# Optimization experiments

Measured on AMD Instinct MI355X. Metric: run time of the kernel, lower is better.

## Reference

```python
import math
import jax, jax.numpy as jnp
import numpy as np


def fht(x):
    """Normalized fast Hadamard transform over the last axis (size = power of 2)."""
    n = x.shape[-1]
    pre = x.shape[:-1]
    y = x.reshape(-1, n)
    h = 1
    while h < n:
        y = y.reshape(-1, n // (2 * h), 2, h)
        a = y[:, :, 0, :]
        b = y[:, :, 1, :]
        y = jnp.stack([a + b, a - b], axis=2)
        h *= 2
    return y.reshape(*pre, n) * jnp.float32(1.0 / math.sqrt(n))


def setup_inputs() -> dict:
    key = jax.random.key(0)
    ks = jax.random.split(key, 8)
    B, N, M, G = 8192, 4096, 4096, 512  # tokens, in_features(n_pad), out_features(m_pad), n_pad//8
    CB = 256  # E8 shell codebook entries (8-bit indices), each an 8-dim lattice point
    x = jax.random.normal(ks[0], (B, N), dtype=jnp.float32)
    Qidxs = jax.random.randint(ks[1], (M, G), 0, CB, dtype=jnp.int32)
    Qidxs2 = jax.random.randint(ks[2], (M, G), 0, CB, dtype=jnp.int32)
    SU = jax.random.rademacher(ks[3], (M,), dtype=jnp.float32)  # row sign vector
    SV = jax.random.rademacher(ks[4], (N,), dtype=jnp.float32)  # column sign vector
    codebook = jax.random.normal(ks[5], (CB, 8), dtype=jnp.float32)
    codebook2 = jax.random.normal(ks[6], (CB, 8), dtype=jnp.float32)
    Wscale = jnp.asarray(0.85, dtype=jnp.float32)
    inv_resid_scale = jnp.asarray(0.07, dtype=jnp.float32)  # nonzero -> stage-2 enabled
    return {"x": x, "Qidxs": Qidxs, "Qidxs2": Qidxs2, "SU": SU, "SV": SV,
            "codebook": codebook, "codebook2": codebook2,
            "Wscale": Wscale, "inv_resid_scale": inv_resid_scale}


def reference(x, Qidxs, Qidxs2, SU, SV, codebook, codebook2, Wscale, inv_resid_scale):
    # in_features == n_pad and out_features == m_pad here (powers of 2), so no pad/slice.
    m_pad, g = Qidxs.shape
    n_pad = g * 8
    # 1) input RHT: signs then Hadamard
    x_rht = fht(x * SV[None, :])  # (B, n_pad)
    # 2) dequantize weights in RHT domain: codebook lookup per 8-dim group + residual stage
    W_rht = codebook[Qidxs].reshape(m_pad, n_pad)
    W_rht = W_rht + codebook2[Qidxs2].reshape(m_pad, n_pad) * inv_resid_scale
    # 3) matmul in RHT domain with global scale
    y_rht = (x_rht @ W_rht.T) * Wscale  # (B, m_pad)
    # 4) output inverse RHT: Hadamard then signs
    y = fht(y_rht) * SU[None, :]
    return y
```

## Files before the change

### kernel.cpp

```cpp
#include <hip/hip_runtime.h>

#define B_DIM 8192
#define N_DIM 4096
#define M_DIM 4096
#define G_DIM 512

typedef short bf16x8 __attribute__((ext_vector_type(8)));
typedef float f32x4 __attribute__((ext_vector_type(4)));

typedef __attribute__((address_space(1))) const void gvoid_t;
typedef __attribute__((address_space(3))) void lvoid_t;

__device__ __forceinline__ void load_lds16(const void* g, void* l) {
    __builtin_amdgcn_global_load_lds((gvoid_t*)g, (lvoid_t*)l, 16, 0, 0);
}

__device__ __forceinline__ unsigned lds_u32(const void* p) {
    return (unsigned)(unsigned long long)(lvoid_t*)p;
}

__device__ __forceinline__ unsigned short f2bf(float f) {
    union { float f; unsigned int u; } v; v.f = f;
    unsigned int u = v.u;
    unsigned int r = (u + 0x7fffu + ((u >> 16) & 1u)) >> 16;
    return (unsigned short)r;
}
__device__ __forceinline__ float bf2f(unsigned short s) {
    union { unsigned int u; float f; } v; v.u = ((unsigned int)s) << 16;
    return v.f;
}

__device__ __forceinline__ void h16(float* v) {
#pragma unroll
    for (int h = 1; h < 16; h <<= 1) {
#pragma unroll
        for (int i = 0; i < 16; i++) {
            if (!(i & h)) {
                float a = v[i], b = v[i | h];
                v[i] = a + b;
                v[i | h] = a - b;
            }
        }
    }
}

__device__ __forceinline__ void h64(float* v) {
#pragma unroll
    for (int h = 1; h < 64; h <<= 1) {
#pragma unroll
        for (int i = 0; i < 64; i++) {
            if (!(i & h)) {
                float a = v[i], b = v[i | h];
                v[i] = a + b;
                v[i | h] = a - b;
            }
        }
    }
}

__global__ __launch_bounds__(256) void k_build_w(
    const int* __restrict__ q1, const int* __restrict__ q2,
    const float* __restrict__ cb1, const float* __restrict__ cb2,
    const float* __restrict__ wsp, const float* __restrict__ irsp,
    unsigned short* __restrict__ W) {
    __shared__ float c1[256 * 9];
    __shared__ float c2[256 * 9];
    int t = threadIdx.x;
#pragma unroll
    for (int j = 0; j < 8; j++) {
        c1[t * 9 + j] = cb1[t * 8 + j];
        c2[t * 9 + j] = cb2[t * 8 + j];
    }
    __syncthreads();
    float ws = wsp[0];
    float irs = irsp[0] * ws;
    int gid = blockIdx.x * 256 + t;
    int i1 = q1[gid] * 9;
    int i2 = q2[gid] * 9;
    union { unsigned short s[8]; int4 v; } o;
#pragma unroll
    for (int j = 0; j < 8; j++) {
        o.s[j] = f2bf(c1[i1 + j] * ws + c2[i2 + j] * irs);
    }
    *(int4*)(W + (size_t)gid * 8) = o.v;
}

__global__ __launch_bounds__(256) void k_hadw(
    unsigned short* __restrict__ W, int base_mul, int step, float scale) {
    int c = blockIdx.x * 256 + threadIdx.x;
    int base = blockIdx.y * base_mul;
    float v[64];
#pragma unroll
    for (int j = 0; j < 64; j++)
        v[j] = bf2f(W[(size_t)(base + j * step) * N_DIM + c]);
    h64(v);
#pragma unroll
    for (int j = 0; j < 64; j++)
        W[(size_t)(base + j * step) * N_DIM + c] = f2bf(v[j] * scale);
}

__global__ __launch_bounds__(256) void k_rht_in(
    const float* __restrict__ x, const float* __restrict__ SV,
    unsigned short* __restrict__ out) {
    __shared__ float lds[4352];
    int row = blockIdx.x;
    int t = threadIdx.x;
    const float* xr = x + (size_t)row * N_DIM;
    float v[16];
#pragma unroll
    for (int r = 0; r < 16; r++) {
        int n = t + (r << 8);
        v[r] = xr[n] * SV[n] * 0.015625f;
    }
    h16(v);
#pragma unroll
    for (int r = 0; r < 16; r++) { int n = t + (r << 8); lds[n + (n >> 4)] = v[r]; }
    __syncthreads();
#pragma unroll
    for (int r = 0; r < 16; r++) { int n = (t << 4) + r; v[r] = lds[n + (n >> 4)]; }
    h16(v);
#pragma unroll
    for (int r = 0; r < 16; r++) { int n = (t << 4) + r; lds[n + (n >> 4)] = v[r]; }
    __syncthreads();
#pragma unroll
    for (int r = 0; r < 16; r++) {
        int n = (t & 15) | (r << 4) | ((t >> 4) << 8);
        v[r] = lds[n + (n >> 4)];
    }
    h16(v);
#pragma unroll
    for (int r = 0; r < 16; r++) {
        int n = (t & 15) | (r << 4) | ((t >> 4) << 8);
        lds[n + (n >> 4)] = v[r];
    }
    __syncthreads();
    unsigned short* orow = out + (size_t)row * N_DIM;
#pragma unroll
    for (int r = 0; r < 16; r++) {
        int n = t + (r << 8);
        orow[n] = f2bf(lds[n + (n >> 4)]);
    }
}

#define DSR(D, A, OFF) \
    asm volatile("ds_read_b128 %0, %1 offset:" #OFF : "=v"(D) : "v"(A))
#define SB0() __builtin_amdgcn_sched_barrier(0)
#define SGB(M, N) __builtin_amdgcn_sched_group_barrier((M), (N), 0)

__global__ __launch_bounds__(512, 2) void k_gemm(
    const unsigned short* __restrict__ A,
    const unsigned short* __restrict__ Bw,
    const float* __restrict__ SU,
    float* __restrict__ C) {
    __shared__ __align__(16) unsigned short lds[4 * 16384];

    int t = threadIdx.x;
    int w = t >> 6;
    int l = t & 63;

    int lin = blockIdx.x;
    int xcd = lin & 7;
    int idx = lin >> 3;
    int bn = xcd * 2 + (idx >> 5);
    int bm = idx & 31;

    int lx = l ^ (l >> 3);
    const unsigned short* aS0 =
        A + (size_t)(bm * 256 + w * 16 + (lx >> 2)) * N_DIM + (lx & 3) * 8;
    const unsigned short* aS1 = aS0 + (size_t)128 * N_DIM;
    const unsigned short* bS0 =
        Bw + (size_t)(bn * 256 + w * 16 + (lx >> 2)) * N_DIM + (lx & 3) * 8;
    const unsigned short* bS1 = bS0 + (size_t)128 * N_DIM;

    int wm = w >> 2;
    int wn = w & 3;
    int quad = l >> 4;
    int ln = l & 15;
    unsigned ldsU = lds_u32(lds);
    unsigned aByte = ldsU +
        (unsigned)(((((wm * 128) + ln) << 6) | (quad << 4)) ^ ((ln >> 1) << 4));
    unsigned bByte = ldsU + 16384u +
        (unsigned)(((((wn * 64) + ln) << 6) | (quad << 4)) ^ ((ln >> 1) << 4));

    f32x4 acc[8][4];
#pragma unroll
    for (int i = 0; i < 8; i++)
#pragma unroll
        for (int j = 0; j < 4; j++) {
            f32x4 z = {0.f, 0.f, 0.f, 0.f};
            acc[i][j] = z;
        }

#define STAGE(KT) do {                                              \
        int kt_ = (KT);                                             \
        int ks_ = kt_ < 127 ? kt_ : 127;                            \
        unsigned short* d_ = lds + ((unsigned)kt_ & 3u) * 16384 + w * 512; \
        load_lds16(aS0 + ks_ * 32, d_);                             \
        load_lds16(aS1 + ks_ * 32, d_ + 4096);                      \
        load_lds16(bS0 + ks_ * 32, d_ + 8192);                      \
        load_lds16(bS1 + ks_ * 32, d_ + 12288);                     \
    } while (0)

#define GROUP(I, BC) do {                                           \
        acc[I][0] = __builtin_amdgcn_mfma_f32_16x16x32_bf16(        \
            af[I], BC[0], acc[I][0], 0, 0, 0);                      \
        acc[I][1] = __builtin_amdgcn_mfma_f32_16x16x32_bf16(        \
            af[I], BC[1], acc[I][1], 0, 0, 0);                      \
        acc[I][2] = __builtin_amdgcn_mfma_f32_16x16x32_bf16(        \
            af[I], BC[2], acc[I][2], 0, 0, 0);                      \
        acc[I][3] = __builtin_amdgcn_mfma_f32_16x16x32_bf16(        \
            af[I], BC[3], acc[I][3], 0, 0, 0);                      \
    } while (0)

#define BODY(K, BC, BN) do {                                        \
        asm volatile("s_waitcnt lgkmcnt(0)");                       \
        SB0();   \
        STAGE((K) + 3);                                             \
        unsigned aun = aByte + ((unsigned)((K) + 1) & 3u) * 32768u; \
        unsigned bun = bByte + ((unsigned)((K) + 1) & 3u) * 32768u; \
        SGB(0x10, 4);                       \
        GROUP(0, BC); DSR(af[0], aun, 0);    DSR(BN[0], bun, 0);    \
        SGB(0x8, 4); SGB(0x100, 2);                                 \
        GROUP(1, BC); DSR(af[1], aun, 1024); DSR(BN[1], bun, 1024); \
        SGB(0x8, 4); SGB(0x100, 2);                                 \
        GROUP(2, BC); DSR(af[2], aun, 2048); DSR(BN[2], bun, 2048); \
        SGB(0x8, 4); SGB(0x100, 2);                                 \
        GROUP(3, BC); DSR(af[3], aun, 3072); DSR(BN[3], bun, 3072); \
        SGB(0x8, 4); SGB(0x100, 2);                                 \
        GROUP(4, BC); DSR(af[4], aun, 4096);                        \
        SGB(0x8, 4); SGB(0x100, 1);                                 \
        GROUP(5, BC); DSR(af[5], aun, 5120);                        \
        SGB(0x8, 4); SGB(0x100, 1);                                 \
        GROUP(6, BC); DSR(af[6], aun, 6144);                        \
        SGB(0x8, 4); SGB(0x100, 1);                                 \
        GROUP(7, BC); DSR(af[7], aun, 7168);                        \
        SGB(0x8, 4); SGB(0x100, 1);                                 \
        asm volatile("s_waitcnt vmcnt(4)");   \
        asm volatile("" ::: "memory");                              \
        __builtin_amdgcn_s_barrier();                               \
        asm volatile("" ::: "memory");                              \
    } while (0)

    bf16x8 af[8], bfrA[4], bfrB[4];

    STAGE(0);
    STAGE(1);
    STAGE(2);
    asm volatile("s_waitcnt vmcnt(4)");
    __builtin_amdgcn_s_barrier();
    asm volatile("" ::: "memory");
    {
        unsigned au0 = aByte;
        unsigned bu0 = bByte;
        DSR(af[0], au0, 0);
        DSR(af[1], au0, 1024);
        DSR(af[2], au0, 2048);
        DSR(af[3], au0, 3072);
        DSR(af[4], au0, 4096);
        DSR(af[5], au0, 5120);
        DSR(af[6], au0, 6144);
        DSR(af[7], au0, 7168);
        DSR(bfrA[0], bu0, 0);
        DSR(bfrA[1], bu0, 1024);
        DSR(bfrA[2], bu0, 2048);
        DSR(bfrA[3], bu0, 3072);
    }

    for (int k = 0; k < N_DIM / 32; k += 2) {
        BODY(k, bfrA, bfrB);
        BODY(k + 1, bfrB, bfrA);
    }
    asm volatile("s_waitcnt vmcnt(0) lgkmcnt(0)");

#pragma unroll
    for (int j = 0; j < 4; j++) {
        int col = bn * 256 + wn * 64 + j * 16 + ln;
        float su = SU[col];
#pragma unroll
        for (int i = 0; i < 8; i++) {
#pragma unroll
            for (int r = 0; r < 4; r++) {
                int rowg = bm * 256 + wm * 128 + i * 16 + quad * 4 + r;
                C[(size_t)rowg * M_DIM + col] = acc[i][j][r] * su;
            }
        }
    }
#undef STAGE
#undef GROUP
#undef BODY
}

extern "C" void kernel_launch(void* const* d_in, const int* in_sizes, int n_in,
                              void* d_out, int out_size, void* d_ws, size_t ws_size,
                              hipStream_t stream) {
    const float* x    = (const float*)d_in[0];
    const int*   q1   = (const int*)d_in[1];
    const int*   q2   = (const int*)d_in[2];
    const float* SU   = (const float*)d_in[3];
    const float* SV   = (const float*)d_in[4];
    const float* cb1  = (const float*)d_in[5];
    const float* cb2  = (const float*)d_in[6];
    const float* wsp  = (const float*)d_in[7];
    const float* irsp = (const float*)d_in[8];
    float* out = (float*)d_out;

    unsigned short* xrht = (unsigned short*)d_ws;
    unsigned short* Wb   = xrht + (size_t)B_DIM * N_DIM;

    k_build_w<<<dim3((M_DIM * G_DIM) / 256), dim3(256), 0, stream>>>(
        q1, q2, cb1, cb2, wsp, irsp, Wb);
    k_hadw<<<dim3(N_DIM / 256, 64), dim3(256), 0, stream>>>(Wb, 1, 64, 1.0f);
    k_hadw<<<dim3(N_DIM / 256, 64), dim3(256), 0, stream>>>(Wb, 64, 1, 0.015625f);
    k_rht_in<<<dim3(B_DIM), dim3(256), 0, stream>>>(x, SV, xrht);
    k_gemm<<<dim3(512), dim3(512), 0, stream>>>(xrht, Wb, SU, out);
}
```

Measured before the change: 521.0 us.

## Fuse weight dequant with first Hadamard pass and tile second pass via LDS

Weight construction now dequantizes a 64-row by 256-column tile into shared memory and applies the low-stride 64-point Hadamard there before writing bf16. This removes one full round trip of the weight matrix through global memory. The remaining high-stride Hadamard pass also stages a tile in LDS with 16-byte vector loads and stores instead of per-element 2-byte accesses. The large shared tile reduces occupancy per CU, and the extra intermediate rounding to bf16 between passes is kept.

```diff
diff --git a/kernel.cpp b/kernel.cpp
--- a/kernel.cpp
+++ b/kernel.cpp
@@ -58,13 +58,14 @@
     }
 }
 
-__global__ __launch_bounds__(256) void k_build_w(
+__global__ __launch_bounds__(256) void k_build_hlo(
     const int* __restrict__ q1, const int* __restrict__ q2,
     const float* __restrict__ cb1, const float* __restrict__ cb2,
     const float* __restrict__ wsp, const float* __restrict__ irsp,
     unsigned short* __restrict__ W) {
     __shared__ float c1[256 * 9];
     __shared__ float c2[256 * 9];
+    __shared__ float tile[64 * 256];
     int t = threadIdx.x;
 #pragma unroll
     for (int j = 0; j < 8; j++) {
@@ -74,29 +75,77 @@
     __syncthreads();
     float ws = wsp[0];
     float irs = irsp[0] * ws;
-    int gid = blockIdx.x * 256 + t;
-    int i1 = q1[gid] * 9;
-    int i2 = q2[gid] * 9;
-    union { unsigned short s[8]; int4 v; } o;
-#pragma unroll
-    for (int j = 0; j < 8; j++) {
-        o.s[j] = f2bf(c1[i1 + j] * ws + c2[i2 + j] * irs);
-    }
-    *(int4*)(W + (size_t)gid * 8) = o.v;
-}
-
-__global__ __launch_bounds__(256) void k_hadw(
-    unsigned short* __restrict__ W, int base_mul, int step, float scale) {
-    int c = blockIdx.x * 256 + threadIdx.x;
-    int base = blockIdx.y * base_mul;
-    float v[64];
-#pragma unroll
-    for (int j = 0; j < 64; j++)
-        v[j] = bf2f(W[(size_t)(base + j * step) * N_DIM + c]);
-    h64(v);
-#pragma unroll
-    for (int j = 0; j < 64; j++)
-        W[(size_t)(base + j * step) * N_DIM + c] = f2bf(v[j] * scale);
+    int ct = blockIdx.x;
+    int h  = blockIdx.y;
+    int g0 = ct * 32;
+    int rr = t >> 5;
+    int j  = t & 31;
+#pragma unroll
+    for (int p = 0; p < 8; p++) {
+        int row = rr + 8 * p;
+        int m = 64 * h + row;
+        int i1 = q1[m * G_DIM + g0 + j] * 9;
+        int i2 = q2[m * G_DIM + g0 + j] * 9;
+        float* dst = &tile[row * 256 + 8 * j];
+#pragma unroll
+        for (int i = 0; i < 8; i++) dst[i] = c1[i1 + i] * ws + c2[i2 + i] * irs;
+    }
+    __syncthreads();
+    {
+        float v[64];
+#pragma unroll
+        for (int r2 = 0; r2 < 64; r2++) v[r2] = tile[r2 * 256 + t];
+        h64(v);
+#pragma unroll
+        for (int r2 = 0; r2 < 64; r2++) tile[r2 * 256 + t] = v[r2];
+    }
+    __syncthreads();
+#pragma unroll
+    for (int p = 0; p < 8; p++) {
+        int row = rr + 8 * p;
+        int m = 64 * h + row;
+        union { unsigned short s[8]; int4 v4; } o;
+#pragma unroll
+        for (int i = 0; i < 8; i++) o.s[i] = f2bf(tile[row * 256 + 8 * j + i]);
+        *(int4*)(W + (size_t)m * N_DIM + ct * 256 + 8 * j) = o.v4;
+    }
+}
+
+__global__ __launch_bounds__(256) void k_hadw_hi(unsigned short* __restrict__ W) {
+    __shared__ float tile[64 * 256];
+    int t = threadIdx.x;
+    int ct = blockIdx.x;
+    int lo = blockIdx.y;
+    int rr = t >> 5;
+    int j = t & 31;
+#pragma unroll
+    for (int p = 0; p < 8; p++) {
+        int hi = rr + 8 * p;
+        size_t m = (size_t)lo + 64 * hi;
+        union { int4 v4; unsigned short s[8]; } u;
+        u.v4 = *(const int4*)(W + m * N_DIM + ct * 256 + 8 * j);
+#pragma unroll
+        for (int i = 0; i < 8; i++) tile[hi * 256 + 8 * j + i] = bf2f(u.s[i]);
+    }
+    __syncthreads();
+    {
+        float v[64];
+#pragma unroll
+        for (int hi = 0; hi < 64; hi++) v[hi] = tile[hi * 256 + t];
+        h64(v);
+#pragma unroll
+        for (int hi = 0; hi < 64; hi++) tile[hi * 256 + t] = v[hi] * 0.015625f;
+    }
+    __syncthreads();
+#pragma unroll
+    for (int p = 0; p < 8; p++) {
+        int hi = rr + 8 * p;
+        size_t m = (size_t)lo + 64 * hi;
+        union { unsigned short s[8]; int4 v4; } o;
+#pragma unroll
+        for (int i = 0; i < 8; i++) o.s[i] = f2bf(tile[hi * 256 + 8 * j + i]);
+        *(int4*)(W + m * N_DIM + ct * 256 + 8 * j) = o.v4;
+    }
 }
 
 __global__ __launch_bounds__(256) void k_rht_in(
@@ -307,10 +356,9 @@
     unsigned short* xrht = (unsigned short*)d_ws;
     unsigned short* Wb   = xrht + (size_t)B_DIM * N_DIM;
 
-    k_build_w<<<dim3((M_DIM * G_DIM) / 256), dim3(256), 0, stream>>>(
+    k_build_hlo<<<dim3(16, 64), dim3(256), 0, stream>>>(
         q1, q2, cb1, cb2, wsp, irsp, Wb);
-    k_hadw<<<dim3(N_DIM / 256, 64), dim3(256), 0, stream>>>(Wb, 1, 64, 1.0f);
-    k_hadw<<<dim3(N_DIM / 256, 64), dim3(256), 0, stream>>>(Wb, 64, 1, 0.015625f);
+    k_hadw_hi<<<dim3(16, 64), dim3(256), 0, stream>>>(Wb);
     k_rht_in<<<dim3(B_DIM), dim3(256), 0, stream>>>(x, SV, xrht);
     k_gemm<<<dim3(512), dim3(512), 0, stream>>>(xrht, Wb, SU, out);
 }
```

After: 529.6 us. Within noise of the previous version (+1.6%).
